# Kernel tuning notes

Measured on AMD Instinct MI355X. Metric: run time of the kernel, lower is better.

The kernel has to match this reference:

```python
import jax, jax.numpy as jnp
import numpy as np

DIM = 1024
SEQ = 2048
HID = 128
HEADS = 8
DECAY_CONST = SEQ // 512  # 4


def setup_inputs() -> dict:
    key = jax.random.key(0)
    ks = jax.random.split(key, 8)
    x = jax.random.normal(ks[0], (8, DIM, SEQ), dtype=jnp.float32)
    # per-head input projections: Linear(dim, hidden_dim)
    proj_w = jax.random.normal(ks[1], (HEADS, HID, DIM), dtype=jnp.float32) / np.sqrt(DIM)
    proj_b = jax.random.normal(ks[2], (HEADS, HID), dtype=jnp.float32) * 0.01
    # mixer params: weight (seq,), bias (seq,), decay_value scalar per head
    mix_w = jax.random.normal(ks[3], (HEADS, SEQ), dtype=jnp.float32)
    mix_b = jnp.zeros((HEADS, SEQ), dtype=jnp.float32)
    decay_v = jnp.ones((HEADS,), dtype=jnp.float32)
    # output projection Linear(dim, dim)
    out_w = jax.random.normal(ks[4], (DIM, DIM), dtype=jnp.float32) / np.sqrt(DIM)
    out_b = jax.random.normal(ks[5], (DIM,), dtype=jnp.float32) * 0.01
    return {"x": x, "proj_w": proj_w, "proj_b": proj_b, "mix_w": mix_w,
            "mix_b": mix_b, "decay_v": decay_v, "out_w": out_w, "out_b": out_b}


def _decay_matrices(mix_w, decay_v):
    """Build per-head upper-triangular decayed matrices M[h] (S,S).
    First HEADS//2 heads: ColRepeat (value v[j] on column j);
    last HEADS//2 heads: RowRepeat (value v[i] on row i).
    Entry (i,j) for j>=i is v * clip(d,0.9,1)**((j-i)/DECAY_CONST)."""
    S = mix_w.shape[1]
    H2 = HEADS // 2
    i = jnp.arange(S)[:, None]
    j = jnp.arange(S)[None, :]
    mask = j >= i                                  # (S,S)
    expo = jnp.where(mask, (j - i) / DECAY_CONST, 0.0).astype(jnp.float32)
    d = jnp.clip(decay_v, 0.9, 1.0)                # (H,)
    dpow = d[:, None, None] ** expo[None]          # (H,S,S)
    col_v = jnp.broadcast_to(mix_w[:H2, None, :], (H2, S, S))   # v[j]
    row_v = jnp.broadcast_to(mix_w[H2:, :, None], (HEADS - H2, S, S))  # v[i]
    vmat = jnp.concatenate([col_v, row_v], axis=0)  # (H,S,S)
    return jnp.where(mask[None], vmat * dpow, 0.0)


def reference(x, proj_w, proj_b, mix_w, mix_b, decay_v, out_w, out_b):
    # x: (B, E=dim, T=seq)
    x_bte = jnp.transpose(x, (0, 2, 1))                       # (B,T,E)
    proj = jnp.einsum('bte,hde->bhtd', x_bte, proj_w) + proj_b[None, :, None, :]  # (B,H,T,D)
    M = _decay_matrices(mix_w, decay_v)                        # (H,S,S)
    # mixer: out[t'] = sum_t proj[t] * M[t, t'] ; bias is added per-time-step
    mixed = jnp.einsum('bhtd,hts->bhsd', proj, M) + mix_b[None, :, :, None]  # (B,H,S,D)
    B, H, S, D = mixed.shape
    hidden = jnp.transpose(mixed, (0, 2, 1, 3)).reshape(B, S, H * D)  # concat heads
    out = hidden @ out_w.T + out_b                             # (B,S,dim)
    return jnp.transpose(out, (0, 2, 1))                       # (B,dim,S)
```

## Files before the change

kernel.cpp:

```cpp
#include <hip/hip_runtime.h>

#define DIM 1024
#define SEQ 2048
#define HID 128
#define HEADS 8
#define DECAYC 4
#define CHUNK 32
#define NCH (SEQ / CHUNK)
#define BK 64
#define NT (DIM / BK)

typedef __bf16 bf16x8 __attribute__((ext_vector_type(8)));
typedef float f32x4 __attribute__((ext_vector_type(4)));
typedef unsigned short u16x4 __attribute__((ext_vector_type(4)));

__device__ __forceinline__ unsigned short f2bf(float f) {
  union { float f; unsigned u; } v; v.f = f;
  unsigned r = v.u + 0x7fffu + ((v.u >> 16) & 1u);
  return (unsigned short)(r >> 16);
}
__device__ __forceinline__ float bf2f(unsigned short u) {
  union { unsigned u; float f; } v; v.u = ((unsigned)u) << 16;
  return v.f;
}

typedef __attribute__((address_space(1))) const unsigned int* g_u32p;
typedef __attribute__((address_space(3))) unsigned int* l_u32p;

__device__ __forceinline__ void async_ld16(const unsigned short* g, unsigned short* l) {
  __builtin_amdgcn_global_load_lds((g_u32p)g, (l_u32p)l, 16, 0, 0);
}

__device__ __forceinline__ int swz(int c) { return c ^ (((c >> 7) & 7) << 4); }

__global__ void convertk(const float* __restrict__ in, unsigned short* __restrict__ out, int n) {
  int i = blockIdx.x * 256 + threadIdx.x;
  if (i < n) out[i] = f2bf(in[i]);
}

__global__ __launch_bounds__(256) void transpose_x(const float* __restrict__ x,
                                                   unsigned short* __restrict__ xT) {
  __shared__ float tile[64][65];
  const int b = blockIdx.z;
  const int e0 = blockIdx.x * 64;
  const int t0 = blockIdx.y * 64;
  const int tr = threadIdx.x >> 6;
  const int tc = threadIdx.x & 63;
  const float* xp = x + ((size_t)b * DIM + e0) * SEQ + t0;
#pragma unroll
  for (int i = 0; i < 16; ++i) {
    int e = i * 4 + tr;
    tile[e][tc] = xp[(size_t)e * SEQ + tc];
  }
  __syncthreads();
  unsigned short* op = xT + ((size_t)b * SEQ + t0) * DIM + e0;
#pragma unroll
  for (int i = 0; i < 16; ++i) {
    int t = i * 4 + tr;
    op[(size_t)t * DIM + tc] = f2bf(tile[tc][t]);
  }
}

template <int C_BF16, int BIAS_ROW, int MODE>
__global__ __launch_bounds__(512, 2) void gemm256(const unsigned short* __restrict__ A,
                                                  const unsigned short* __restrict__ B,
                                                  void* __restrict__ Cv,
                                                  const float* __restrict__ bias,
                                                  int ldc, long sB, long sC) {
  __shared__ unsigned short lds[65536];

  int m0, n0, z;
  if constexpr (MODE == 1) {
    m0 = (blockIdx.x >> 2) * 256;
    n0 = (blockIdx.x & 3) * 256;
    z = 0;
  } else {
    z = blockIdx.x >> 5;
    m0 = ((blockIdx.x >> 3) & 3) * 256;
    n0 = (blockIdx.x & 7) * 256;
  }
  B += (size_t)sB * z;

  const int tid = threadIdx.x;
  const int lane = tid & 63;
  const int w = tid >> 6;
  const int wm = w >> 2;
  const int wn = w & 3;

  const unsigned short* srcA[4];
  const unsigned short* srcB[4];
#pragma unroll
  for (int j = 0; j < 4; ++j) {
    int c = (w * 4 + j) * 1024 + lane * 16;
    int cs = swz(c);
    int row = cs >> 7;
    int kk = (cs & 127) >> 1;
    srcA[j] = A + (size_t)(m0 + row) * DIM + kk;
    srcB[j] = B + (size_t)(n0 + row) * DIM + kk;
  }

  const int r15 = lane & 15;
  const int hi16 = (lane >> 4) * 16;
  int aoff[8][2], boff[4][2];
#pragma unroll
  for (int fi = 0; fi < 8; ++fi)
#pragma unroll
    for (int ks = 0; ks < 2; ++ks)
      aoff[fi][ks] = swz((wm * 128 + fi * 16 + r15) * 128 + ks * 64 + hi16) >> 1;
#pragma unroll
  for (int fj = 0; fj < 4; ++fj)
#pragma unroll
    for (int ks = 0; ks < 2; ++ks)
      boff[fj][ks] = swz((wn * 64 + fj * 16 + r15) * 128 + ks * 64 + hi16) >> 1;

  f32x4 acc[8][4] = {};

#define STAGE(t, d)                                                     \
  {                                                                     \
    const int kt_ = (t) * BK;                                           \
    unsigned short* base_ = (unsigned short*)lds + (d) * 32768;         \
    _Pragma("unroll") for (int j = 0; j < 4; ++j)                       \
        async_ld16(srcA[j] + kt_, base_ + (w * 4 + j) * 512);           \
    _Pragma("unroll") for (int j = 0; j < 4; ++j)                       \
        async_ld16(srcB[j] + kt_, base_ + 16384 + (w * 4 + j) * 512);   \
  }

  STAGE(0, 0);
  int cur = 0;
  for (int t = 0; t < NT; ++t) {
    if (t + 1 < NT) {
      STAGE(t + 1, cur ^ 1);
      asm volatile("s_waitcnt vmcnt(8)" ::: "memory");
    } else {
      asm volatile("s_waitcnt vmcnt(0)" ::: "memory");
    }
    __builtin_amdgcn_s_barrier();
    asm volatile("" ::: "memory");
    {
      const unsigned short* ba = (const unsigned short*)lds + cur * 32768;
      const unsigned short* bb = ba + 16384;
#pragma unroll
      for (int q = 0; q < 4; ++q) {
        const int ks = q & 1;
        const int g = (q >> 1) * 4;
        bf16x8 af[4], bfr[4];
#pragma unroll
        for (int i = 0; i < 4; ++i) af[i] = *(const bf16x8*)&ba[aoff[g + i][ks]];
#pragma unroll
        for (int j = 0; j < 4; ++j) bfr[j] = *(const bf16x8*)&bb[boff[j][ks]];
        __builtin_amdgcn_s_setprio(1);
#pragma unroll
        for (int i = 0; i < 4; ++i)
#pragma unroll
          for (int j = 0; j < 4; ++j)
            acc[g + i][j] =
                __builtin_amdgcn_mfma_f32_16x16x32_bf16(af[i], bfr[j], acc[g + i][j], 0, 0, 0);
        __builtin_amdgcn_s_setprio(0);
      }
    }
    asm volatile("" ::: "memory");
    __builtin_amdgcn_s_barrier();
    cur ^= 1;
  }

  const int or0 = (lane >> 4) * 4;
#pragma unroll
  for (int fi = 0; fi < 8; ++fi) {
#pragma unroll
    for (int fj = 0; fj < 4; ++fj) {
      const int col = n0 + wn * 64 + fj * 16 + r15;
      const int rowb = m0 + wm * 128 + fi * 16 + or0;
      float cb = BIAS_ROW ? 0.0f : bias[col];
#pragma unroll
      for (int q = 0; q < 4; ++q) {
        const int row = rowb + q;
        float v = acc[fi][fj][q] + (BIAS_ROW ? bias[row] : cb);
        if constexpr (C_BF16) {
          ((unsigned short*)Cv)[(size_t)sC * z + (size_t)row * ldc + col] = f2bf(v);
        } else {
          ((float*)Cv)[(size_t)sC * z + (size_t)row * ldc + col] = v;
        }
      }
    }
  }
#undef STAGE
}

__global__ __launch_bounds__(256) void scan_carry(const unsigned short* __restrict__ proj,
                                                  float* __restrict__ carry,
                                                  const float* __restrict__ mix_w,
                                                  const float* __restrict__ decay_v) {
  const int b = blockIdx.x >> 6;
  const int c = blockIdx.x & (NCH - 1);
  const int n0 = threadIdx.x * 4;
  const int h = n0 >> 7;
  const float d = fminf(fmaxf(decay_v[h], 0.9f), 1.0f);
  const float r = powf(d, 1.0f / (float)DECAYC);
  const bool colrep = h < (HEADS / 2);
  const u16x4* p = (const u16x4*)(proj + ((size_t)(b * SEQ + c * CHUNK)) * DIM + n0);
  const float* mw = mix_w + h * SEQ + c * CHUNK;
  float s0 = 0.f, s1 = 0.f, s2 = 0.f, s3 = 0.f;
#pragma unroll 8
  for (int t = 0; t < CHUNK; ++t) {
    u16x4 v = p[t * (DIM / 4)];
    float wi = colrep ? 1.0f : mw[t];
    s0 = s0 * r + bf2f(v[0]) * wi;
    s1 = s1 * r + bf2f(v[1]) * wi;
    s2 = s2 * r + bf2f(v[2]) * wi;
    s3 = s3 * r + bf2f(v[3]) * wi;
  }
  f32x4 out = {s0, s1, s2, s3};
  *(f32x4*)(carry + ((size_t)(b * NCH + c)) * DIM + n0) = out;
}

__global__ __launch_bounds__(256) void scan_prefix(float* __restrict__ carry,
                                                   const float* __restrict__ decay_v) {
  const int idx = blockIdx.x * 256 + threadIdx.x;
  const int b = idx >> 10;
  const int n = idx & 1023;
  const int h = n >> 7;
  const float d = fminf(fmaxf(decay_v[h], 0.9f), 1.0f);
  const float r = powf(d, 1.0f / (float)DECAYC);
  const float rL = powf(r, (float)CHUNK);
  float P = 0.0f;
  for (int c = 0; c < NCH; ++c) {
    float* p = carry + ((size_t)(b * NCH + c)) * DIM + n;
    float cc = *p;
    *p = P;
    P = rL * P + cc;
  }
}

__global__ __launch_bounds__(256) void scan_apply(const unsigned short* __restrict__ proj,
                                                  unsigned short* __restrict__ hidden,
                                                  const float* __restrict__ carry,
                                                  const float* __restrict__ mix_w,
                                                  const float* __restrict__ mix_b,
                                                  const float* __restrict__ decay_v) {
  const int b = blockIdx.x >> 6;
  const int c = blockIdx.x & (NCH - 1);
  const int n0 = threadIdx.x * 4;
  const int h = n0 >> 7;
  const float d = fminf(fmaxf(decay_v[h], 0.9f), 1.0f);
  const float r = powf(d, 1.0f / (float)DECAYC);
  const bool colrep = h < (HEADS / 2);
  const size_t base = ((size_t)(b * SEQ + c * CHUNK)) * DIM + n0;
  const u16x4* p = (const u16x4*)(proj + base);
  u16x4* o = (u16x4*)(hidden + base);
  const float* mw = mix_w + h * SEQ + c * CHUNK;
  const float* mb = mix_b + h * SEQ + c * CHUNK;
  f32x4 ci = *(const f32x4*)(carry + ((size_t)(b * NCH + c)) * DIM + n0);
  float s0 = ci[0], s1 = ci[1], s2 = ci[2], s3 = ci[3];
#pragma unroll 8
  for (int t = 0; t < CHUNK; ++t) {
    u16x4 v = p[t * (DIM / 4)];
    float wv = mw[t];
    float wi = colrep ? 1.0f : wv;
    float wo = colrep ? wv : 1.0f;
    float bb = mb[t];
    s0 = s0 * r + bf2f(v[0]) * wi;
    s1 = s1 * r + bf2f(v[1]) * wi;
    s2 = s2 * r + bf2f(v[2]) * wi;
    s3 = s3 * r + bf2f(v[3]) * wi;
    u16x4 ov;
    ov[0] = f2bf(s0 * wo + bb);
    ov[1] = f2bf(s1 * wo + bb);
    ov[2] = f2bf(s2 * wo + bb);
    ov[3] = f2bf(s3 * wo + bb);
    o[t * (DIM / 4)] = ov;
  }
}

extern "C" void kernel_launch(void* const* d_in, const int* in_sizes, int n_in,
                              void* d_out, int out_size, void* d_ws, size_t ws_size,
                              hipStream_t stream) {
  const float* x = (const float*)d_in[0];
  const float* proj_w = (const float*)d_in[1];
  const float* proj_b = (const float*)d_in[2];
  const float* mix_w = (const float*)d_in[3];
  const float* mix_b = (const float*)d_in[4];
  const float* decay_v = (const float*)d_in[5];
  const float* out_w = (const float*)d_in[6];
  const float* out_b = (const float*)d_in[7];

  char* ws = (char*)d_ws;
  unsigned short* xT = (unsigned short*)ws;
  unsigned short* proj = (unsigned short*)(ws + 33554432);
  unsigned short* W1 = (unsigned short*)(ws + 67108864);
  unsigned short* W2 = (unsigned short*)(ws + 69206016);
  unsigned short* hidden = xT;
  float* carryf = (float*)(ws + 67108864);

  const int NW = DIM * DIM;
  convertk<<<dim3((NW + 255) / 256), 256, 0, stream>>>(proj_w, W1, NW);
  convertk<<<dim3((NW + 255) / 256), 256, 0, stream>>>(out_w, W2, NW);
  transpose_x<<<dim3(16, 32, 8), 256, 0, stream>>>(x, xT);

  gemm256<1, 0, 1><<<dim3(256), 512, 0, stream>>>(xT, W1, proj, proj_b, DIM, 0L, 0L);

  scan_carry<<<dim3(8 * NCH), 256, 0, stream>>>(proj, carryf, mix_w, decay_v);
  scan_prefix<<<dim3(8192 / 256), 256, 0, stream>>>(carryf, decay_v);
  scan_apply<<<dim3(8 * NCH), 256, 0, stream>>>(proj, hidden, carryf, mix_w, mix_b, decay_v);

  gemm256<0, 1, 2><<<dim3(256), 512, 0, stream>>>(W2, hidden, d_out, out_b, SEQ,
                                                  (long)SEQ * DIM, (long)DIM * SEQ);
}
```

Measured before the change: 130.8 us.

## Split GEMM K-tile into half-tiles with finer-grained interleaved prefetch schedule

Reorganizes the LDS layout of the bf16 GEMM so each 64-wide K tile is stored as two 32-wide halves with a new XOR swizzle. The main loop becomes four phases, each issuing part of the next tile's async global->LDS loads between fragment reads and MFMA blocks, with barriers between phases. The goal is to overlap memory traffic with compute more evenly and reduce LDS bank conflicts. It adds more barriers per tile and the loads run two tiles ahead within a double buffer, which makes correctness depend on tight phase ordering.

After: 129.5 us. About the same (-1.0%).

```diff
diff --git a/kernel.cpp b/kernel.cpp
--- a/kernel.cpp
+++ b/kernel.cpp
@@ -31,8 +31,6 @@
   __builtin_amdgcn_global_load_lds((g_u32p)g, (l_u32p)l, 16, 0, 0);
 }
 
-__device__ __forceinline__ int swz(int c) { return c ^ (((c >> 7) & 7) << 4); }
-
 __global__ void convertk(const float* __restrict__ in, unsigned short* __restrict__ out, int n) {
   int i = blockIdx.x * 256 + threadIdx.x;
   if (i < n) out[i] = f2bf(in[i]);
@@ -87,83 +85,89 @@
   const int wm = w >> 2;
   const int wn = w & 3;
 
-  const unsigned short* srcA[4];
-  const unsigned short* srcB[4];
-#pragma unroll
-  for (int j = 0; j < 4; ++j) {
-    int c = (w * 4 + j) * 1024 + lane * 16;
-    int cs = swz(c);
-    int row = cs >> 7;
-    int kk = (cs & 127) >> 1;
-    srcA[j] = A + (size_t)(m0 + row) * DIM + kk;
-    srcB[j] = B + (size_t)(n0 + row) * DIM + kk;
+  const unsigned short* sp[2][2][2];
+#pragma unroll
+  for (int j = 0; j < 2; ++j) {
+    int c = (w * 2 + j) * 1024 + lane * 16;
+    int cs = c ^ (((c >> 7) & 3) << 4);
+    int row = cs >> 6;
+    int colel = (cs & 63) >> 1;
+#pragma unroll
+    for (int kh = 0; kh < 2; ++kh) {
+      sp[0][kh][j] = A + (size_t)(m0 + row) * DIM + kh * 32 + colel;
+      sp[1][kh][j] = B + (size_t)(n0 + row) * DIM + kh * 32 + colel;
+    }
   }
 
   const int r15 = lane & 15;
-  const int hi16 = (lane >> 4) * 16;
+  const int hi = lane >> 4;
+  const int rsw = ((r15 >> 1) & 3) << 4;
   int aoff[8][2], boff[4][2];
 #pragma unroll
-  for (int fi = 0; fi < 8; ++fi)
-#pragma unroll
-    for (int ks = 0; ks < 2; ++ks)
-      aoff[fi][ks] = swz((wm * 128 + fi * 16 + r15) * 128 + ks * 64 + hi16) >> 1;
-#pragma unroll
-  for (int fj = 0; fj < 4; ++fj)
-#pragma unroll
-    for (int ks = 0; ks < 2; ++ks)
-      boff[fj][ks] = swz((wn * 64 + fj * 16 + r15) * 128 + ks * 64 + hi16) >> 1;
+  for (int fi = 0; fi < 8; ++fi) {
+    int byte = ((wm * 128 + fi * 16 + r15) * 64 + hi * 16) ^ rsw;
+#pragma unroll
+    for (int ks = 0; ks < 2; ++ks) aoff[fi][ks] = ks * 8192 + (byte >> 1);
+  }
+#pragma unroll
+  for (int fj = 0; fj < 4; ++fj) {
+    int byte = ((wn * 64 + fj * 16 + r15) * 64 + hi * 16) ^ rsw;
+#pragma unroll
+    for (int ks = 0; ks < 2; ++ks) boff[fj][ks] = 16384 + ks * 8192 + (byte >> 1);
+  }
 
   f32x4 acc[8][4] = {};
 
-#define STAGE(t, d)                                                     \
-  {                                                                     \
-    const int kt_ = (t) * BK;                                           \
-    unsigned short* base_ = (unsigned short*)lds + (d) * 32768;         \
-    _Pragma("unroll") for (int j = 0; j < 4; ++j)                       \
-        async_ld16(srcA[j] + kt_, base_ + (w * 4 + j) * 512);           \
-    _Pragma("unroll") for (int j = 0; j < 4; ++j)                       \
-        async_ld16(srcB[j] + kt_, base_ + 16384 + (w * 4 + j) * 512);   \
-  }
-
-  STAGE(0, 0);
-  int cur = 0;
+#define STG(dd, op, kh, tgt)                                                    \
+  if ((tgt) < NT) {                                                             \
+    unsigned short* dst_ = (unsigned short*)lds + (dd) * 32768 + (op) * 16384 + \
+                           (kh) * 8192 + w * 1024;                              \
+    async_ld16(sp[op][kh][0] + (tgt) * BK, dst_);                               \
+    async_ld16(sp[op][kh][1] + (tgt) * BK, dst_ + 512);                         \
+  }
+
+#define PHASE(H_, KS_, MIDBAR, STAGE_STMT)                                      \
+  {                                                                             \
+    bf16x8 af[4], bfr[4];                                                       \
+    _Pragma("unroll") for (int i = 0; i < 4; ++i)                               \
+        af[i] = *(const bf16x8*)&lb[aoff[(H_) * 4 + i][KS_]];                   \
+    _Pragma("unroll") for (int j = 0; j < 4; ++j)                               \
+        bfr[j] = *(const bf16x8*)&lb[boff[j][KS_]];                             \
+    STAGE_STMT;                                                                 \
+    if (MIDBAR) __builtin_amdgcn_s_barrier();                                   \
+    asm volatile("s_waitcnt lgkmcnt(0)" ::: "memory");                          \
+    __builtin_amdgcn_sched_barrier(0);                                          \
+    __builtin_amdgcn_s_setprio(1);                                              \
+    _Pragma("unroll") for (int i = 0; i < 4; ++i)                               \
+      _Pragma("unroll") for (int j = 0; j < 4; ++j)                             \
+        acc[(H_) * 4 + i][j] = __builtin_amdgcn_mfma_f32_16x16x32_bf16(         \
+            af[i], bfr[j], acc[(H_) * 4 + i][j], 0, 0, 0);                      \
+    __builtin_amdgcn_s_setprio(0);                                              \
+    __builtin_amdgcn_s_barrier();                                               \
+  }
+
+  STG(0, 0, 0, 0); STG(0, 1, 0, 0); STG(0, 0, 1, 0); STG(0, 1, 1, 0);
+  STG(1, 0, 0, 1); STG(1, 1, 0, 1);
+
+#pragma unroll
   for (int t = 0; t < NT; ++t) {
-    if (t + 1 < NT) {
-      STAGE(t + 1, cur ^ 1);
-      asm volatile("s_waitcnt vmcnt(8)" ::: "memory");
+    const int d = t & 1;
+    const unsigned short* lb = (const unsigned short*)lds + d * 32768;
+    if (t == NT - 1) {
+      asm volatile("s_waitcnt vmcnt(0)" ::: "memory");
     } else {
-      asm volatile("s_waitcnt vmcnt(0)" ::: "memory");
+      asm volatile("s_waitcnt vmcnt(4)" ::: "memory");
     }
     __builtin_amdgcn_s_barrier();
-    asm volatile("" ::: "memory");
-    {
-      const unsigned short* ba = (const unsigned short*)lds + cur * 32768;
-      const unsigned short* bb = ba + 16384;
-#pragma unroll
-      for (int q = 0; q < 4; ++q) {
-        const int ks = q & 1;
-        const int g = (q >> 1) * 4;
-        bf16x8 af[4], bfr[4];
-#pragma unroll
-        for (int i = 0; i < 4; ++i) af[i] = *(const bf16x8*)&ba[aoff[g + i][ks]];
-#pragma unroll
-        for (int j = 0; j < 4; ++j) bfr[j] = *(const bf16x8*)&bb[boff[j][ks]];
-        __builtin_amdgcn_s_setprio(1);
-#pragma unroll
-        for (int i = 0; i < 4; ++i)
-#pragma unroll
-          for (int j = 0; j < 4; ++j)
-            acc[g + i][j] =
-                __builtin_amdgcn_mfma_f32_16x16x32_bf16(af[i], bfr[j], acc[g + i][j], 0, 0, 0);
-        __builtin_amdgcn_s_setprio(0);
-      }
-    }
-    asm volatile("" ::: "memory");
-    __builtin_amdgcn_s_barrier();
-    cur ^= 1;
-  }
-
-  const int or0 = (lane >> 4) * 4;
+    PHASE(0, 0, 0, STG(d ^ 1, 0, 1, t + 1));
+    PHASE(1, 0, 1, STG(d ^ 1, 1, 1, t + 1));
+    PHASE(0, 1, 1, STG(d, 0, 0, t + 2));
+    PHASE(1, 1, 1, STG(d, 1, 0, t + 2));
+  }
+#undef PHASE
+#undef STG
+
+  const int or0 = hi * 4;
 #pragma unroll
   for (int fi = 0; fi < 8; ++fi) {
 #pragma unroll
@@ -183,7 +187,6 @@
       }
     }
   }
-#undef STAGE
 }
 
 __global__ __launch_bounds__(256) void scan_carry(const unsigned short* __restrict__ proj,
```
